# Optimization experiments

Measured on AMD Instinct MI355X. Metric: run time of the kernel, lower is better.

## Reference

```python
import jax, jax.numpy as jnp
import numpy as np

N = 50000        # points
NN = 32          # neighbors per point
K = 15           # kernel points (KPConv default)
D_IN = 64        # backbone channels
D_OUT = 1024     # feeds Linear(1024, 512)
B = 16           # point clouds in the batch
SIGMA = 0.3      # kernel influence radius


def setup_inputs() -> dict:
    key = jax.random.key(0)
    ks = jax.random.split(key, 12)
    pos = jax.random.normal(ks[0], (N, 3), jnp.float32)
    feats = jax.random.normal(ks[1], (N, D_IN), jnp.float32)
    # kernel points roughly inside the influence sphere
    kernel_points = jax.random.normal(ks[2], (K, 3), jnp.float32) * 0.2
    kp_weights = jax.random.normal(ks[3], (K, D_IN, D_OUT), jnp.float32) / np.sqrt(K * D_IN)
    w1 = jax.random.normal(ks[4], (1024, 512), jnp.float32) / np.sqrt(1024)
    b1 = jnp.zeros((512,), jnp.float32)
    w2 = jax.random.normal(ks[5], (512, 256), jnp.float32) / np.sqrt(512)
    b2 = jnp.zeros((256,), jnp.float32)
    w3 = jax.random.normal(ks[6], (256, 152), jnp.float32) / np.sqrt(256)
    b3 = jnp.zeros((152,), jnp.float32)
    neighbor_idx = jax.random.randint(ks[7], (N, NN), 0, N, jnp.int32)
    batch = jnp.sort(jax.random.randint(ks[8], (N,), 0, B, jnp.int32))
    return {"pos": pos, "feats": feats, "kernel_points": kernel_points,
            "kp_weights": kp_weights, "w1": w1, "b1": b1, "w2": w2, "b2": b2,
            "w3": w3, "b3": b3, "neighbor_idx": neighbor_idx, "batch": batch}


def reference(pos, feats, kernel_points, kp_weights, w1, b1, w2, b2, w3, b3,
              neighbor_idx, batch):
    # --- KPConv: gather neighbors, kernel-point correlation, aggregate ---
    rel = pos[neighbor_idx] - pos[:, None, :]                 # [N, NN, 3]
    # distance of each relative neighbor position to each kernel point
    d = jnp.linalg.norm(rel[:, :, None, :] - kernel_points[None, None], axis=-1)  # [N, NN, K]
    h = jnp.maximum(0.0, 1.0 - d / SIGMA)                     # linear correlation
    nbr_f = feats[neighbor_idx]                               # [N, NN, D_IN] gather
    g = jnp.einsum('njk,njd->nkd', h, nbr_f)                  # per-kernel aggregate
    x = jnp.einsum('nkd,kdo->no', g, kp_weights)              # [N, D_OUT]
    x = jax.nn.leaky_relu(x, 0.1)
    # --- global_mean_pool over batch ids ---
    pooled_sum = jax.ops.segment_sum(x, batch, num_segments=B)            # [B, D_OUT]
    counts = jax.ops.segment_sum(jnp.ones((x.shape[0], 1), x.dtype), batch,
                                 num_segments=B)
    pooled = pooled_sum / jnp.maximum(counts, 1.0)
    h1 = jax.nn.relu(pooled @ w1 + b1)
    h2 = jax.nn.relu(h1 @ w2 + b2)
    return h2 @ w3 + b3                                        # [B, 152]
```

## Files before the change

### kernel.cpp

```cpp
#include <hip/hip_runtime.h>
#include <hip/hip_bf16.h>

#define N_PTS 50000
#define NNB   32
#define KP    15
#define DIN   64
#define DOUT  1024
#define KDIM  (KP*DIN)
#define NB    16
#define SIGMA_INV (1.0f/0.3f)

#define BM 64
#define BN 64
#define BK 64
#define NKT (KDIM/BK)
#define RB_FULL 784
#define NCB (DOUT/BN)
#define NWG (RB_FULL*NCB)
#define NSEG 196
#define WT_BLOCKS 240

typedef __attribute__((ext_vector_type(8))) short bf16x8;
typedef __attribute__((ext_vector_type(4))) float f32x4;

#define GLD16(gsrc, ldst) \
  __builtin_amdgcn_global_load_lds((const __attribute__((address_space(1))) char*)(gsrc), \
                                   (__attribute__((address_space(3))) char*)(ldst), 16, 0, 0)

__global__ __launch_bounds__(256) void prep_kernel(
    const float* __restrict__ W, __hip_bfloat16* __restrict__ Wt,
    const float* __restrict__ pos, const float* __restrict__ feats,
    const float* __restrict__ kpts, const int* __restrict__ nidx,
    __hip_bfloat16* __restrict__ g, int* __restrict__ flag,
    int* __restrict__ bcnt) {
  __shared__ union {
    float t[64][65];
    struct { float h[4][16][33]; int cnts; } kc;
  } sm;
  int tid = threadIdx.x;
  if (blockIdx.x < WT_BLOCKS) {
    int i = blockIdx.x;
    int k0 = (i % 15) * 64;
    int o0 = (i / 15) * 64;
    int tx = tid & 63, ty = tid >> 6;
    for (int r = ty; r < 64; r += 4) sm.t[r][tx] = W[(size_t)(k0 + r)*DOUT + o0 + tx];
    __syncthreads();
    for (int r = ty; r < 64; r += 4)
      Wt[(size_t)(o0 + r)*KDIM + k0 + tx] = __float2bfloat16(sm.t[tx][r]);
    return;
  }
  int w = tid >> 6, lane = tid & 63;
  if (tid == 0) sm.kc.cnts = 0;
  __syncthreads();
  int n = (blockIdx.x - WT_BLOCKS) * 4 + w;
  if (n < N_PTS) {
    int myj = lane & 31;
    int khalf = lane >> 5;
    int id0 = nidx[n*NNB + myj];
    float px = pos[n*3+0], py = pos[n*3+1], pz = pos[n*3+2];
    float rx = pos[id0*3+0] - px;
    float ry = pos[id0*3+1] - py;
    float rz = pos[id0*3+2] - pz;
    bool anyact = false;
    float hreg[8];
    #pragma unroll
    for (int i = 0; i < 8; ++i) {
      int k = 2*i + khalf;
      float h = 0.0f;
      if (k < KP) {
        float dx = rx - kpts[k*3+0];
        float dy = ry - kpts[k*3+1];
        float dz = rz - kpts[k*3+2];
        float d = sqrtf(dx*dx + dy*dy + dz*dz);
        h = 1.0f - d * SIGMA_INV;
        h = h > 0.0f ? h : 0.0f;
        anyact |= (h > 0.0f);
      }
      hreg[i] = h;
    }
    unsigned long long bal = __ballot(anyact);
    if (bal) {
      unsigned int actj = (unsigned int)(bal | (bal >> 32));
      if ((actj >> myj) & 1) {
        #pragma unroll
        for (int i = 0; i < 8; ++i) {
          int k = 2*i + khalf;
          if (k < KP) sm.kc.h[w][k][myj] = hreg[i];
        }
      }
      float acc[KP];
      #pragma unroll
      for (int k = 0; k < KP; ++k) acc[k] = 0.0f;
      while (actj) {
        int j = __ffs(actj) - 1;
        actj &= actj - 1;
        int id = __shfl(id0, j);
        float f = feats[(size_t)id*DIN + lane];
        #pragma unroll
        for (int k = 0; k < KP; ++k) acc[k] += sm.kc.h[w][k][j] * f;
      }
      size_t base = (size_t)n*KDIM;
      #pragma unroll
      for (int k = 0; k < KP; ++k)
        g[base + k*DIN + lane] = __float2bfloat16(acc[k]);
    }
    if (lane == 0) {
      int active = (bal != 0ull) ? 1 : 0;
      flag[n] = active;
      if (active) atomicAdd(&sm.kc.cnts, 1);
    }
  }
  __syncthreads();
  if (tid == 0 && sm.kc.cnts) atomicAdd(&bcnt[(blockIdx.x - WT_BLOCKS) >> 6], sm.kc.cnts);
}

__global__ __launch_bounds__(256) void fill_kernel(
    const int* __restrict__ flag, const int* __restrict__ bcnt,
    const int* __restrict__ batch, int* __restrict__ rowlist,
    int* __restrict__ bidc, int* __restrict__ mact) {
  __shared__ int s[256];
  __shared__ int boff_l;
  int tid = threadIdx.x;
  int bc = (tid < NSEG) ? bcnt[tid] : 0;
  s[tid] = (tid < (int)blockIdx.x) ? bc : 0;
  __syncthreads();
  for (int d = 1; d < 256; d <<= 1) {
    int v = (tid >= d) ? s[tid-d] : 0;
    __syncthreads();
    s[tid] += v;
    __syncthreads();
  }
  if (tid == 255) boff_l = s[255];
  __syncthreads();
  int boff = boff_l;
  int n = blockIdx.x*256 + tid;
  int f = (n < N_PTS) ? flag[n] : 0;
  s[tid] = f;
  __syncthreads();
  for (int d = 1; d < 256; d <<= 1) {
    int v = (tid >= d) ? s[tid-d] : 0;
    __syncthreads();
    s[tid] += v;
    __syncthreads();
  }
  if (f) {
    int sl = boff + s[tid] - 1;
    rowlist[sl] = n;
    bidc[sl] = batch[n];
  }
  if (blockIdx.x == NSEG-1 && tid == 255) *mact = boff + s[255];
}

__global__ __launch_bounds__(256) void gemm_mfma_pool(
    const __hip_bfloat16* __restrict__ g, const __hip_bfloat16* __restrict__ Wt,
    const int* __restrict__ rowlist, const int* __restrict__ bidc,
    const int* __restrict__ mact, float* __restrict__ partial) {
  __shared__ __align__(16) char lA[BM*128];
  __shared__ __align__(16) char lB[BN*128];
  __shared__ float psum[NB][BN];
  __shared__ int bid[BM];
  int wg = blockIdx.x;
  int xg = wg & 7, t = wg >> 3;
  int rb = ((t >> 4) << 3) + xg;
  int cb = t & 15;
  int Ma = *mact;
  int r0 = rb*BM, c0 = cb*BN;
  int tid = threadIdx.x;
  if (r0 >= Ma) return;
  int lane = tid & 63, w = tid >> 6;
  int wr = w >> 1, wc = w & 1;

  int gc = (tid & 7) ^ ((tid >> 3) & 7);
  const __hip_bfloat16* pA[2];
  #pragma unroll
  for (int i = 0; i < 2; ++i) {
    int slot = r0 + i*32 + (tid >> 3);
    int rl = (slot < Ma) ? rowlist[slot] : 0;
    pA[i] = g + (size_t)rl*KDIM + gc*8;
  }
  const __hip_bfloat16* pB[2];
  #pragma unroll
  for (int i = 0; i < 2; ++i)
    pB[i] = Wt + (size_t)(c0 + i*32 + (tid >> 3))*KDIM + gc*8;

  if (tid < BM) bid[tid] = (r0 + tid < Ma) ? bidc[r0 + tid] : -1;
  for (int z = tid; z < NB*BN; z += 256) (&psum[0][0])[z] = 0.0f;

  f32x4 acc[2][2] = {};

  for (int kt = 0; kt < NKT; ++kt) {
    int k0 = kt*BK;
    #pragma unroll
    for (int i = 0; i < 2; ++i) GLD16(pA[i] + k0, lA + (i*256 + tid)*16);
    #pragma unroll
    for (int i = 0; i < 2; ++i) GLD16(pB[i] + k0, lB + (i*256 + tid)*16);
    __syncthreads();
    #pragma unroll
    for (int ks = 0; ks < 2; ++ks) {
      bf16x8 af[2], bfr[2];
      #pragma unroll
      for (int m = 0; m < 2; ++m) {
        int row = wr*32 + m*16 + (lane & 15);
        int ch = (ks*4 + (lane >> 4)) ^ (row & 7);
        af[m] = *(const bf16x8*)(lA + row*128 + ch*16);
      }
      #pragma unroll
      for (int n = 0; n < 2; ++n) {
        int row = wc*32 + n*16 + (lane & 15);
        int ch = (ks*4 + (lane >> 4)) ^ (row & 7);
        bfr[n] = *(const bf16x8*)(lB + row*128 + ch*16);
      }
      #pragma unroll
      for (int m = 0; m < 2; ++m)
        #pragma unroll
        for (int n = 0; n < 2; ++n)
          acc[m][n] = __builtin_amdgcn_mfma_f32_16x16x32_bf16(af[m], bfr[n], acc[m][n], 0, 0, 0);
    }
    __syncthreads();
  }

  int q = lane >> 4;
  #pragma unroll 1
  for (int phase = 0; phase < 8; ++phase) {
    if (wr*4 + q == phase) {
      #pragma unroll
      for (int n = 0; n < 2; ++n) {
        int c = wc*32 + n*16 + (lane & 15);
        float run = 0.0f; int curb = -2;
        #pragma unroll
        for (int m = 0; m < 2; ++m) {
          #pragma unroll
          for (int j = 0; j < 4; ++j) {
            int r = wr*32 + m*16 + q*4 + j;
            int b = bid[r];
            float v = acc[m][n][j];
            v = v > 0.0f ? v : 0.1f*v;
            if (b != curb) { if (curb >= 0) psum[curb][c] += run; run = 0.0f; curb = b; }
            run += v;
          }
        }
        if (curb >= 0) psum[curb][c] += run;
      }
    }
    __syncthreads();
  }
  int bmin = bid[0];
  int lastv = (r0 + BM <= Ma) ? (BM-1) : (Ma - 1 - r0);
  int bmax = bid[lastv];
  int nbw = bmax - bmin + 1;
  for (int z = tid; z < nbw*BN; z += 256) {
    int bo = z >> 6, c = z & 63;
    partial[((size_t)rb*NB + bmin + bo)*DOUT + c0 + c] = psum[bmin + bo][c];
  }
}

__global__ __launch_bounds__(512) void mlpA_kernel(
    const float* __restrict__ partial, const int* __restrict__ batch,
    const int* __restrict__ bidc, const int* __restrict__ mact,
    const float* __restrict__ w1, float* __restrict__ part1) {
  __shared__ float red[16][128];
  __shared__ float pl[128];
  __shared__ float h1p[4][512];
  int s = blockIdx.x, b = blockIdx.y, t = threadIdx.x;
  int Ma = *mact;
  int clb, cub;
  { int l = 0, r = Ma; while (l < r) { int m = (l+r)>>1; if (bidc[m] <  b) l = m+1; else r = m; } clb = l; }
  { int l = 0, r = Ma; while (l < r) { int m = (l+r)>>1; if (bidc[m] <= b) l = m+1; else r = m; } cub = l; }
  int rb0 = clb >> 6;
  int rb1 = (cub > clb) ? ((cub - 1) >> 6) : (rb0 - 1);
  {
    int seg = t >> 5, q = t & 31;
    float4 v = {0.f, 0.f, 0.f, 0.f};
    for (int rb = rb0 + seg; rb <= rb1; rb += 16) {
      const float4 p = *(const float4*)&partial[((size_t)rb*NB + b)*DOUT + s*128 + q*4];
      v.x += p.x; v.y += p.y; v.z += p.z; v.w += p.w;
    }
    *(float4*)&red[seg][q*4] = v;
  }
  __syncthreads();
  if (t < 128) {
    float sum = 0.0f;
    #pragma unroll
    for (int e = 0; e < 16; ++e) sum += red[e][t];
    int lb, ub;
    { int l = 0, r = N_PTS; while (l < r) { int m = (l+r)>>1; if (batch[m] <  b) l = m+1; else r = m; } lb = l; }
    { int l = 0, r = N_PTS; while (l < r) { int m = (l+r)>>1; if (batch[m] <= b) l = m+1; else r = m; } ub = l; }
    pl[t] = sum / fmaxf((float)(ub - lb), 1.0f);
  }
  __syncthreads();
  {
    int oq = t & 127, kseg = t >> 7;
    float4 a = {0.f, 0.f, 0.f, 0.f};
    #pragma unroll 8
    for (int i = 0; i < 32; ++i) {
      int k = kseg*32 + i;
      float p = pl[k];
      const float4 wv = *(const float4*)&w1[(size_t)(s*128 + k)*512 + oq*4];
      a.x += p*wv.x; a.y += p*wv.y; a.z += p*wv.z; a.w += p*wv.w;
    }
    *(float4*)&h1p[kseg][oq*4] = a;
  }
  __syncthreads();
  float r1 = (h1p[0][t] + h1p[1][t]) + (h1p[2][t] + h1p[3][t]);
  part1[((size_t)b*8 + s)*512 + t] = r1;
}

__global__ __launch_bounds__(512) void mlpBC_kernel(
    const float* __restrict__ part1, const float* __restrict__ b1,
    const float* __restrict__ w2, const float* __restrict__ b2,
    const float* __restrict__ w3, const float* __restrict__ b3,
    float* __restrict__ out) {
  __shared__ float hs[512];
  __shared__ float h2p[8][256];
  __shared__ float h2l[256];
  __shared__ float o3p[8][152];
  int b = blockIdx.x, t = threadIdx.x;
  {
    float v = b1[t];
    #pragma unroll
    for (int s = 0; s < 8; ++s) v += part1[((size_t)b*8 + s)*512 + t];
    hs[t] = fmaxf(v, 0.0f);
  }
  __syncthreads();
  {
    int oq = t & 63, kseg = t >> 6;
    float4 a = {0.f, 0.f, 0.f, 0.f};
    #pragma unroll 8
    for (int i = 0; i < 64; ++i) {
      int j = kseg*64 + i;
      float p = hs[j];
      const float4 wv = *(const float4*)&w2[(size_t)j*256 + oq*4];
      a.x += p*wv.x; a.y += p*wv.y; a.z += p*wv.z; a.w += p*wv.w;
    }
    *(float4*)&h2p[kseg][oq*4] = a;
  }
  __syncthreads();
  if (t < 256) {
    float v = b2[t];
    #pragma unroll
    for (int e = 0; e < 8; ++e) v += h2p[e][t];
    h2l[t] = fmaxf(v, 0.0f);
  }
  __syncthreads();
  if (t < 304) {
    int oq = t % 38, kseg = t / 38;
    float4 a = {0.f, 0.f, 0.f, 0.f};
    #pragma unroll 8
    for (int i = 0; i < 32; ++i) {
      int j = kseg*32 + i;
      float p = h2l[j];
      const float4 wv = *(const float4*)&w3[(size_t)j*152 + oq*4];
      a.x += p*wv.x; a.y += p*wv.y; a.z += p*wv.z; a.w += p*wv.w;
    }
    *(float4*)&o3p[kseg][oq*4] = a;
  }
  __syncthreads();
  if (t < 152) {
    float v = b3[t];
    #pragma unroll
    for (int e = 0; e < 8; ++e) v += o3p[e][t];
    out[b*152 + t] = v;
  }
}

extern "C" void kernel_launch(void* const* d_in, const int* in_sizes, int n_in,
                              void* d_out, int out_size, void* d_ws, size_t ws_size,
                              hipStream_t stream) {
  (void)in_sizes; (void)n_in; (void)out_size; (void)ws_size;
  const float* pos   = (const float*)d_in[0];
  const float* feats = (const float*)d_in[1];
  const float* kpts  = (const float*)d_in[2];
  const float* kpw   = (const float*)d_in[3];
  const float* w1    = (const float*)d_in[4];
  const float* b1    = (const float*)d_in[5];
  const float* w2    = (const float*)d_in[6];
  const float* b2    = (const float*)d_in[7];
  const float* w3    = (const float*)d_in[8];
  const float* b3    = (const float*)d_in[9];
  const int* nidx    = (const int*)d_in[10];
  const int* batch   = (const int*)d_in[11];
  float* out = (float*)d_out;

  char* ws = (char*)d_ws;
  const size_t off_g        = 0;
  const size_t off_bidc     = 96000000;
  const size_t off_rowlist  = off_bidc + 200704;
  const size_t off_flag     = off_rowlist + 200704;
  const size_t off_bcnt     = off_flag + 200704;
  const size_t off_mact     = off_bcnt + 1024;
  const size_t off_wt       = off_mact + 64;
  const size_t off_partial  = off_wt + 1966080;
  const size_t off_p1       = off_partial + 51380224;
  __hip_bfloat16* g  = (__hip_bfloat16*)(ws + off_g);
  int* bidc    = (int*)(ws + off_bidc);
  int* rowlist = (int*)(ws + off_rowlist);
  int* flag    = (int*)(ws + off_flag);
  int* bcnt    = (int*)(ws + off_bcnt);
  int* mact    = (int*)(ws + off_mact);
  __hip_bfloat16* wt = (__hip_bfloat16*)(ws + off_wt);
  float* partial = (float*)(ws + off_partial);
  float* part1   = (float*)(ws + off_p1);

  hipMemsetAsync(bcnt, 0, 1024, stream);
  prep_kernel<<<WT_BLOCKS + (N_PTS+3)/4, 256, 0, stream>>>(
      kpw, wt, pos, feats, kpts, nidx, g, flag, bcnt);
  fill_kernel<<<NSEG, 256, 0, stream>>>(flag, bcnt, batch, rowlist, bidc, mact);
  gemm_mfma_pool<<<NWG, 256, 0, stream>>>(g, wt, rowlist, bidc, mact, partial);
  mlpA_kernel<<<dim3(8, NB), 512, 0, stream>>>(partial, batch, bidc, mact, w1, part1);
  mlpBC_kernel<<<NB, 512, 0, stream>>>(part1, b1, w2, b2, w3, b3, out);
}
```

Before: 152.9 us.

## Split pooling and MLP into batched kernels that share weight tiles

The fused pool+layer1 and layer2+3 kernels are replaced by four kernels: a per-batch pooling reduction, a layer-1 kernel that tiles w1 and processes all 16 batch rows per block, a layer-2 kernel that tiles w2 across batches, and a small layer-3 kernel. The aim is to read each MLP weight once for all batch rows instead of once per batch item. In exchange there are two extra launches and more round trips through global memory, and the pooling kernel now reduces each segment serially with only 16 blocks.

```diff
diff --git a/kernel.cpp b/kernel.cpp
--- a/kernel.cpp
+++ b/kernel.cpp
@@ -254,93 +254,93 @@
   }
 }
 
-__global__ __launch_bounds__(512) void mlpA_kernel(
+__global__ __launch_bounds__(256) void pooled_kernel(
     const float* __restrict__ partial, const int* __restrict__ batch,
     const int* __restrict__ bidc, const int* __restrict__ mact,
-    const float* __restrict__ w1, float* __restrict__ part1) {
-  __shared__ float red[16][128];
-  __shared__ float pl[128];
-  __shared__ float h1p[4][512];
-  int s = blockIdx.x, b = blockIdx.y, t = threadIdx.x;
+    float* __restrict__ pooled) {
+  int b = blockIdx.x, t = threadIdx.x;
   int Ma = *mact;
   int clb, cub;
   { int l = 0, r = Ma; while (l < r) { int m = (l+r)>>1; if (bidc[m] <  b) l = m+1; else r = m; } clb = l; }
   { int l = 0, r = Ma; while (l < r) { int m = (l+r)>>1; if (bidc[m] <= b) l = m+1; else r = m; } cub = l; }
   int rb0 = clb >> 6;
   int rb1 = (cub > clb) ? ((cub - 1) >> 6) : (rb0 - 1);
-  {
-    int seg = t >> 5, q = t & 31;
-    float4 v = {0.f, 0.f, 0.f, 0.f};
-    for (int rb = rb0 + seg; rb <= rb1; rb += 16) {
-      const float4 p = *(const float4*)&partial[((size_t)rb*NB + b)*DOUT + s*128 + q*4];
-      v.x += p.x; v.y += p.y; v.z += p.z; v.w += p.w;
-    }
-    *(float4*)&red[seg][q*4] = v;
-  }
-  __syncthreads();
-  if (t < 128) {
-    float sum = 0.0f;
-    #pragma unroll
-    for (int e = 0; e < 16; ++e) sum += red[e][t];
-    int lb, ub;
-    { int l = 0, r = N_PTS; while (l < r) { int m = (l+r)>>1; if (batch[m] <  b) l = m+1; else r = m; } lb = l; }
-    { int l = 0, r = N_PTS; while (l < r) { int m = (l+r)>>1; if (batch[m] <= b) l = m+1; else r = m; } ub = l; }
-    pl[t] = sum / fmaxf((float)(ub - lb), 1.0f);
-  }
-  __syncthreads();
-  {
-    int oq = t & 127, kseg = t >> 7;
-    float4 a = {0.f, 0.f, 0.f, 0.f};
-    #pragma unroll 8
-    for (int i = 0; i < 32; ++i) {
-      int k = kseg*32 + i;
-      float p = pl[k];
-      const float4 wv = *(const float4*)&w1[(size_t)(s*128 + k)*512 + oq*4];
-      a.x += p*wv.x; a.y += p*wv.y; a.z += p*wv.z; a.w += p*wv.w;
-    }
-    *(float4*)&h1p[kseg][oq*4] = a;
-  }
-  __syncthreads();
-  float r1 = (h1p[0][t] + h1p[1][t]) + (h1p[2][t] + h1p[3][t]);
-  part1[((size_t)b*8 + s)*512 + t] = r1;
-}
-
-__global__ __launch_bounds__(512) void mlpBC_kernel(
+  float4 v = {0.f, 0.f, 0.f, 0.f};
+  for (int rb = rb0; rb <= rb1; ++rb) {
+    const float4 p = *(const float4*)&partial[((size_t)rb*NB + b)*DOUT + t*4];
+    v.x += p.x; v.y += p.y; v.z += p.z; v.w += p.w;
+  }
+  int lb, ub;
+  { int l = 0, r = N_PTS; while (l < r) { int m = (l+r)>>1; if (batch[m] <  b) l = m+1; else r = m; } lb = l; }
+  { int l = 0, r = N_PTS; while (l < r) { int m = (l+r)>>1; if (batch[m] <= b) l = m+1; else r = m; } ub = l; }
+  float inv = 1.0f / fmaxf((float)(ub - lb), 1.0f);
+  v.x *= inv; v.y *= inv; v.z *= inv; v.w *= inv;
+  *(float4*)&pooled[(size_t)b*DOUT + t*4] = v;
+}
+
+__global__ __launch_bounds__(256) void mlp1_kernel(
+    const float* __restrict__ pooled, const float* __restrict__ w1,
+    float* __restrict__ part1) {
+  __shared__ float w1t[256][16];
+  __shared__ float pld[16][256];
+  int kseg = blockIdx.x, oc = blockIdx.y, tid = threadIdx.x;
+  int k0 = kseg*256, o0 = oc*16;
+  #pragma unroll
+  for (int i = 0; i < 4; ++i) {
+    int idx = i*256 + tid;
+    int row = idx >> 2, qc = idx & 3;
+    *(float4*)&w1t[row][qc*4] = *(const float4*)&w1[(size_t)(k0 + row)*512 + o0 + qc*4];
+  }
+  #pragma unroll
+  for (int i = 0; i < 4; ++i) {
+    int idx = i*256 + tid;
+    int b = idx >> 6, q = idx & 63;
+    *(float4*)&pld[b][q*4] = *(const float4*)&pooled[(size_t)b*DOUT + k0 + q*4];
+  }
+  __syncthreads();
+  int b = tid >> 4, o = tid & 15;
+  float acc = 0.0f;
+  #pragma unroll 8
+  for (int k = 0; k < 256; ++k) acc += pld[b][k] * w1t[k][o];
+  part1[((size_t)kseg*NB + b)*512 + o0 + o] = acc;
+}
+
+__global__ __launch_bounds__(256) void mlp2_kernel(
     const float* __restrict__ part1, const float* __restrict__ b1,
     const float* __restrict__ w2, const float* __restrict__ b2,
-    const float* __restrict__ w3, const float* __restrict__ b3,
-    float* __restrict__ out) {
-  __shared__ float hs[512];
-  __shared__ float h2p[8][256];
+    float* __restrict__ h2) {
+  __shared__ float h1l[16][512];
+  __shared__ float w2t[512][16];
+  int oc = blockIdx.x, tid = threadIdx.x;
+  int o0 = oc*16;
+  for (int i = 0; i < 32; ++i) {
+    int idx = i*256 + tid;
+    int b = idx >> 9, j = idx & 511;
+    float v = b1[j] + ((part1[((size_t)0*NB + b)*512 + j] + part1[((size_t)1*NB + b)*512 + j])
+                     + (part1[((size_t)2*NB + b)*512 + j] + part1[((size_t)3*NB + b)*512 + j]));
+    h1l[b][j] = fmaxf(v, 0.0f);
+  }
+  #pragma unroll
+  for (int i = 0; i < 8; ++i) {
+    int idx = i*256 + tid;
+    int row = idx >> 2, qc = idx & 3;
+    *(float4*)&w2t[row][qc*4] = *(const float4*)&w2[(size_t)row*256 + o0 + qc*4];
+  }
+  __syncthreads();
+  int b = tid >> 4, o = tid & 15;
+  float acc = 0.0f;
+  #pragma unroll 8
+  for (int j = 0; j < 512; ++j) acc += h1l[b][j] * w2t[j][o];
+  h2[(size_t)b*256 + o0 + o] = fmaxf(acc + b2[o0 + o], 0.0f);
+}
+
+__global__ __launch_bounds__(512) void mlp3_kernel(
+    const float* __restrict__ h2, const float* __restrict__ w3,
+    const float* __restrict__ b3, float* __restrict__ out) {
   __shared__ float h2l[256];
   __shared__ float o3p[8][152];
   int b = blockIdx.x, t = threadIdx.x;
-  {
-    float v = b1[t];
-    #pragma unroll
-    for (int s = 0; s < 8; ++s) v += part1[((size_t)b*8 + s)*512 + t];
-    hs[t] = fmaxf(v, 0.0f);
-  }
-  __syncthreads();
-  {
-    int oq = t & 63, kseg = t >> 6;
-    float4 a = {0.f, 0.f, 0.f, 0.f};
-    #pragma unroll 8
-    for (int i = 0; i < 64; ++i) {
-      int j = kseg*64 + i;
-      float p = hs[j];
-      const float4 wv = *(const float4*)&w2[(size_t)j*256 + oq*4];
-      a.x += p*wv.x; a.y += p*wv.y; a.z += p*wv.z; a.w += p*wv.w;
-    }
-    *(float4*)&h2p[kseg][oq*4] = a;
-  }
-  __syncthreads();
-  if (t < 256) {
-    float v = b2[t];
-    #pragma unroll
-    for (int e = 0; e < 8; ++e) v += h2p[e][t];
-    h2l[t] = fmaxf(v, 0.0f);
-  }
+  if (t < 256) h2l[t] = h2[(size_t)b*256 + t];
   __syncthreads();
   if (t < 304) {
     int oq = t % 38, kseg = t / 38;
@@ -390,7 +390,9 @@
   const size_t off_mact     = off_bcnt + 1024;
   const size_t off_wt       = off_mact + 64;
   const size_t off_partial  = off_wt + 1966080;
-  const size_t off_p1       = off_partial + 51380224;
+  const size_t off_pooled   = off_partial + 51380224;
+  const size_t off_p1       = off_pooled + 65536;
+  const size_t off_h2       = off_p1 + 131072;
   __hip_bfloat16* g  = (__hip_bfloat16*)(ws + off_g);
   int* bidc    = (int*)(ws + off_bidc);
   int* rowlist = (int*)(ws + off_rowlist);
@@ -399,13 +401,17 @@
   int* mact    = (int*)(ws + off_mact);
   __hip_bfloat16* wt = (__hip_bfloat16*)(ws + off_wt);
   float* partial = (float*)(ws + off_partial);
+  float* pooled  = (float*)(ws + off_pooled);
   float* part1   = (float*)(ws + off_p1);
+  float* h2      = (float*)(ws + off_h2);
 
   hipMemsetAsync(bcnt, 0, 1024, stream);
   prep_kernel<<<WT_BLOCKS + (N_PTS+3)/4, 256, 0, stream>>>(
       kpw, wt, pos, feats, kpts, nidx, g, flag, bcnt);
   fill_kernel<<<NSEG, 256, 0, stream>>>(flag, bcnt, batch, rowlist, bidc, mact);
   gemm_mfma_pool<<<NWG, 256, 0, stream>>>(g, wt, rowlist, bidc, mact, partial);
-  mlpA_kernel<<<dim3(8, NB), 512, 0, stream>>>(partial, batch, bidc, mact, w1, part1);
-  mlpBC_kernel<<<NB, 512, 0, stream>>>(part1, b1, w2, b2, w3, b3, out);
-}
+  pooled_kernel<<<NB, 256, 0, stream>>>(partial, batch, bidc, mact, pooled);
+  mlp1_kernel<<<dim3(4, 32), 256, 0, stream>>>(pooled, w1, part1);
+  mlp2_kernel<<<NB, 256, 0, stream>>>(part1, b1, w2, b2, h2);
+  mlp3_kernel<<<NB, 512, 0, stream>>>(h2, w3, b3, out);
+}
```

Measured after the change: 165.7 us. 1.08x slower.
